# Kernel tuning notes

Measured on AMD Instinct MI355X. Metric: run time of the kernel, lower is better.

The kernel has to match this reference:

```python
import jax, jax.numpy as jnp
import numpy as np

B, S, E, H = 4, 1024, 1024, 16
D = E // H  # head dim = 64

def setup_inputs() -> dict:
    key = jax.random.key(0)
    k1, k2, k3, k4, k5 = jax.random.split(key, 5)
    return {
        "lstm_out": jax.random.normal(k1, (B, S, E), dtype=jnp.float32),
        "in_proj_weight": jax.random.normal(k2, (3 * E, E), dtype=jnp.float32) * 0.02,
        "in_proj_bias": jax.random.normal(k3, (3 * E,), dtype=jnp.float32) * 0.02,
        "out_proj_weight": jax.random.normal(k4, (E, E), dtype=jnp.float32) * 0.02,
        "out_proj_bias": jax.random.normal(k5, (E,), dtype=jnp.float32) * 0.02,
    }

def reference(lstm_out, in_proj_weight, in_proj_bias, out_proj_weight, out_proj_bias):
    # Packed QKV projection, as in nn.MultiheadAttention (Linear uses x @ W.T + b)
    qkv = lstm_out @ in_proj_weight.T + in_proj_bias          # [B,S,3E]
    q, k, v = jnp.split(qkv, 3, axis=-1)                      # each [B,S,E]
    def heads(t):
        return t.reshape(B, S, H, D).transpose(0, 2, 1, 3)    # [B,H,S,D]
    q, k, v = heads(q), heads(k), heads(v)
    scale = 1.0 / jnp.sqrt(jnp.asarray(D, dtype=q.dtype))
    scores = jnp.einsum("bhsd,bhtd->bhst", q * scale, k)      # [B,H,S,S]
    attn = jax.nn.softmax(scores, axis=-1)                    # [B,H,S,S]
    ctx = jnp.einsum("bhst,bhtd->bhsd", attn, v)              # [B,H,S,D]
    ctx = ctx.transpose(0, 2, 1, 3).reshape(B, S, E)          # [B,S,E]
    attn_output = ctx @ out_proj_weight.T + out_proj_bias     # [B,S,E]
    # need_weights=True with default average_attn_weights=True -> mean over heads
    attn_weights = attn.mean(axis=1)                          # [B,S,S]
    context_vector = attn_output.mean(axis=1)                 # [B,E]
    return (context_vector, attn_weights)
```

## Files before the change

### kernel.cpp

```cpp
#include <hip/hip_runtime.h>


typedef unsigned short u16;
using s16x8 = __attribute__((ext_vector_type(8))) short;
using f32x4 = __attribute__((ext_vector_type(4))) float;
using u16x4 = __attribute__((ext_vector_type(4))) unsigned short;

#define AS1 __attribute__((address_space(1)))
#define AS3 __attribute__((address_space(3)))

#define QSCALE 0.1803368801111204f

__device__ __forceinline__ u16 f2bf(float f) {
    unsigned u = __float_as_uint(f);
    u += 0x7fffu + ((u >> 16) & 1u);
    return (u16)(u >> 16);
}

__global__ void k_prep(const float* __restrict__ X, const float* __restrict__ W1,
                       const float* __restrict__ W2, const float* __restrict__ bout,
                       u16* __restrict__ Xb, u16* __restrict__ W1b, u16* __restrict__ W2b,
                       float* __restrict__ out) {
    int i = blockIdx.x * blockDim.x + threadIdx.x;
    const float* src; u16* dst; int off;
    if (i < 1048576)       { src = X;  dst = Xb;  off = i; }
    else if (i < 1835008)  { src = W1; dst = W1b; off = i - 1048576; }
    else                   { src = W2; dst = W2b; off = i - 1835008; }
    float4 v = reinterpret_cast<const float4*>(src)[off];
    u16x4 o = { f2bf(v.x), f2bf(v.y), f2bf(v.z), f2bf(v.w) };
    reinterpret_cast<u16x4*>(dst)[off] = o;
    if (i < 4096) out[i] = bout[i & 1023];
}

template<int MODE>
__global__ __launch_bounds__(512) void k_gemm_bt(
    const u16* __restrict__ A, const u16* __restrict__ B,
    const float* __restrict__ bias, u16* __restrict__ C,
    u16* __restrict__ vt, float* __restrict__ outvec) {
    const int K = 1024;
    constexpr int KSLICE = (MODE == 0) ? 1024 : 256;
    const int nbx = gridDim.x;
    const int nwg = nbx * gridDim.y;
    const int bid = blockIdx.y * nbx + blockIdx.x;
    const int per = nwg >> 3;
    const int swz = (bid & 7) * per + (bid >> 3);
    const int n0 = (swz % nbx) * 128, m0 = (swz / nbx) * 128;
    const int kbeg = blockIdx.z * KSLICE, kend = kbeg + KSLICE;
    const int tid = threadIdx.x, lane = tid & 63, w = tid >> 6;
    const int wm = w >> 1, wn = w & 1;
    const int g = lane >> 4, l15 = lane & 15;
    __shared__ __attribute__((aligned(16))) u16 As[2][128 * 64];
    __shared__ __attribute__((aligned(16))) u16 Bs[2][128 * 64];

    f32x4 acc[2][4];
    #pragma unroll
    for (int mi = 0; mi < 2; ++mi)
        #pragma unroll
        for (int nj = 0; nj < 4; ++nj) acc[mi][nj] = (f32x4){0.f, 0.f, 0.f, 0.f};

    auto STAGE = [&](int k0, int sb) {
        #pragma unroll
        for (int r = 0; r < 2; ++r) {
            int c = tid + r * 512;
            int row = c >> 3, j = c & 7;
            int js = j ^ (row & 7);
            __builtin_amdgcn_global_load_lds(
                (AS1 const void*)(A + (size_t)(m0 + row) * K + k0 + js * 8),
                (AS3 void*)(&As[sb][c * 8]), 16, 0, 0);
            __builtin_amdgcn_global_load_lds(
                (AS1 const void*)(B + (size_t)(n0 + row) * K + k0 + js * 8),
                (AS3 void*)(&Bs[sb][c * 8]), 16, 0, 0);
        }
    };

    STAGE(kbeg, 0);
    int buf = 0;
    for (int k0 = kbeg; k0 < kend; k0 += 64) {
        __syncthreads();
        if (k0 + 64 < kend) STAGE(k0 + 64, buf ^ 1);
        #pragma unroll
        for (int kk = 0; kk < 64; kk += 32) {
            const int cx0 = (((kk >> 3) + g) ^ (l15 & 7)) * 8;
            s16x8 av[2], bv[4];
            #pragma unroll
            for (int mi = 0; mi < 2; ++mi)
                av[mi] = *reinterpret_cast<const s16x8*>(
                    &As[buf][(wm * 32 + mi * 16 + l15) * 64 + cx0]);
            #pragma unroll
            for (int nj = 0; nj < 4; ++nj)
                bv[nj] = *reinterpret_cast<const s16x8*>(
                    &Bs[buf][(wn * 64 + nj * 16 + l15) * 64 + cx0]);
            #pragma unroll
            for (int mi = 0; mi < 2; ++mi)
                #pragma unroll
                for (int nj = 0; nj < 4; ++nj)
                    acc[mi][nj] = __builtin_amdgcn_mfma_f32_16x16x32_bf16(av[mi], bv[nj], acc[mi][nj], 0, 0, 0);
        }
        buf ^= 1;
    }

    if constexpr (MODE == 0) {
        #pragma unroll
        for (int nj = 0; nj < 4; ++nj) {
            int n = n0 + wn * 64 + nj * 16 + l15;
            float scale = (n < 1024) ? QSCALE : 1.0f;
            float bvs = bias[n] * scale;
            if (n < 2048) {
                #pragma unroll
                for (int mi = 0; mi < 2; ++mi)
                    #pragma unroll
                    for (int i = 0; i < 4; ++i) {
                        int m = m0 + wm * 32 + mi * 16 + g * 4 + i;
                        C[(size_t)m * 2048 + n] = f2bf(acc[mi][nj][i] * scale + bvs);
                    }
            } else {
                int hd = n - 2048;
                #pragma unroll
                for (int mi = 0; mi < 2; ++mi)
                    #pragma unroll
                    for (int i = 0; i < 4; ++i) {
                        int m = m0 + wm * 32 + mi * 16 + g * 4 + i;
                        int b = m >> 10, t = m & 1023;
                        vt[((size_t)(b * 16 + (hd >> 6)) * 64 + (hd & 63)) * 1024 + t] =
                            f2bf(acc[mi][nj][i] + bvs);
                    }
            }
        }
    } else {
        int b = m0 >> 10;
        #pragma unroll
        for (int nj = 0; nj < 4; ++nj) {
            float s = 0.f;
            #pragma unroll
            for (int mi = 0; mi < 2; ++mi)
                #pragma unroll
                for (int i = 0; i < 4; ++i) s += acc[mi][nj][i];
            s += __shfl_xor(s, 16);
            s += __shfl_xor(s, 32);
            if (g == 0) {
                int n = n0 + wn * 64 + nj * 16 + l15;
                atomicAdd(&outvec[b * 1024 + n], s * (1.0f / 1024.0f));
            }
        }
    }
}

__global__ __launch_bounds__(256, 4) void k_flash(const u16* __restrict__ qk,
                                                  const u16* __restrict__ vt,
                                                  u16* __restrict__ ctx,
                                                  float* __restrict__ ml) {
    const int id = blockIdx.x + 16 * (blockIdx.y + 16 * blockIdx.z);
    const int x = id & 7, kq = id >> 3;
    const int gbh = x * 8 + (kq >> 4);
    const int qt = kq & 15;
    const int b = gbh >> 4, h = gbh & 15;
    const int q0 = qt * 64;
    const int tid = threadIdx.x, lane = tid & 63, w = tid >> 6;
    const int g = lane >> 4, l15 = lane & 15;
    __shared__ __attribute__((aligned(16))) u16 Ks[2][64 * 64];
    __shared__ __attribute__((aligned(16))) u16 Vt[2][64 * 64];
    __shared__ __attribute__((aligned(16))) u16 Ps[4][16 * 64];

    const size_t rowQ = (size_t)(b * 1024 + q0 + w * 16 + l15) * 2048 + h * 64;
    const s16x8 qa0 = *reinterpret_cast<const s16x8*>(qk + rowQ + g * 8);
    const s16x8 qa1 = *reinterpret_cast<const s16x8*>(qk + rowQ + 32 + g * 8);

    const int cA = tid, cB = tid + 256;
    const int rowA = cA >> 3, jA = cA & 7, rowB = cB >> 3, jB = cB & 7;
    const u16* kbase0 = qk + (size_t)(b * 1024) * 2048 + 1024 + h * 64;
    const u16* vtb = vt + (size_t)(b * 16 + h) * 65536;

    __builtin_amdgcn_global_load_lds((AS1 const void*)(kbase0 + (size_t)rowA * 2048 + ((jA ^ (rowA & 7)) * 8)),
                                     (AS3 void*)(&Ks[0][cA * 8]), 16, 0, 0);
    __builtin_amdgcn_global_load_lds((AS1 const void*)(kbase0 + (size_t)rowB * 2048 + ((jB ^ (rowB & 7)) * 8)),
                                     (AS3 void*)(&Ks[0][cB * 8]), 16, 0, 0);
    __builtin_amdgcn_global_load_lds((AS1 const void*)(vtb + (size_t)rowA * 1024 + ((jA ^ (rowA & 7)) * 8)),
                                     (AS3 void*)(&Vt[0][cA * 8]), 16, 0, 0);
    __builtin_amdgcn_global_load_lds((AS1 const void*)(vtb + (size_t)rowB * 1024 + ((jB ^ (rowB & 7)) * 8)),
                                     (AS3 void*)(&Vt[0][cB * 8]), 16, 0, 0);

    f32x4 ctxa[4];
    #pragma unroll
    for (int nj = 0; nj < 4; ++nj) ctxa[nj] = (f32x4){0.f, 0.f, 0.f, 0.f};
    float lsum = 0.f;

    int buf = 0;
    for (int kt = 0; kt < 16; ++kt) {
        __syncthreads();
        if (kt < 15) {
            int t0n = (kt + 1) * 64;
            const u16* kbase = kbase0 + (size_t)t0n * 2048;
            __builtin_amdgcn_global_load_lds((AS1 const void*)(kbase + (size_t)rowA * 2048 + ((jA ^ (rowA & 7)) * 8)),
                                             (AS3 void*)(&Ks[buf ^ 1][cA * 8]), 16, 0, 0);
            __builtin_amdgcn_global_load_lds((AS1 const void*)(kbase + (size_t)rowB * 2048 + ((jB ^ (rowB & 7)) * 8)),
                                             (AS3 void*)(&Ks[buf ^ 1][cB * 8]), 16, 0, 0);
            const u16* vbase = vtb + t0n;
            __builtin_amdgcn_global_load_lds((AS1 const void*)(vbase + (size_t)rowA * 1024 + ((jA ^ (rowA & 7)) * 8)),
                                             (AS3 void*)(&Vt[buf ^ 1][cA * 8]), 16, 0, 0);
            __builtin_amdgcn_global_load_lds((AS1 const void*)(vbase + (size_t)rowB * 1024 + ((jB ^ (rowB & 7)) * 8)),
                                             (AS3 void*)(&Vt[buf ^ 1][cB * 8]), 16, 0, 0);
        }

        f32x4 sc[4];
        #pragma unroll
        for (int tj = 0; tj < 4; ++tj) sc[tj] = (f32x4){0.f, 0.f, 0.f, 0.f};
        __builtin_amdgcn_s_setprio(1);
        #pragma unroll
        for (int kk = 0; kk < 64; kk += 32) {
            s16x8 qa = kk ? qa1 : qa0;
            #pragma unroll
            for (int tj = 0; tj < 4; ++tj) {
                int trow = tj * 16 + l15;
                s16x8 kb = *reinterpret_cast<const s16x8*>(
                    &Ks[buf][trow * 64 + ((((kk >> 3) + g) ^ (trow & 7)) * 8)]);
                sc[tj] = __builtin_amdgcn_mfma_f32_16x16x32_bf16(kb, qa, sc[tj], 0, 0, 0);
            }
        }
        __builtin_amdgcn_s_setprio(0);

        #pragma unroll
        for (int tj = 0; tj < 4; ++tj)
            #pragma unroll
            for (int i = 0; i < 4; ++i) {
                float p = exp2f(sc[tj][i]);
                sc[tj][i] = p;
                lsum += p;
            }

        #pragma unroll
        for (int tj = 0; tj < 4; ++tj) {
            unsigned pk01, pk23;
            asm("v_cvt_pk_bf16_f32 %0, %1, %2" : "=v"(pk01) : "v"(sc[tj][0]), "v"(sc[tj][1]));
            asm("v_cvt_pk_bf16_f32 %0, %1, %2" : "=v"(pk23) : "v"(sc[tj][2]), "v"(sc[tj][3]));
            uint2 pk = { pk01, pk23 };
            *reinterpret_cast<uint2*>(
                &Ps[w][l15 * 64 + (((tj * 2 + (g >> 1)) ^ (l15 & 7)) * 8) + (g & 1) * 4]) = pk;
        }

        __builtin_amdgcn_s_setprio(1);
        #pragma unroll
        for (int kk = 0; kk < 64; kk += 32) {
            s16x8 pa = *reinterpret_cast<const s16x8*>(
                &Ps[w][l15 * 64 + ((((kk >> 3) + g) ^ (l15 & 7)) * 8)]);
            #pragma unroll
            for (int nj = 0; nj < 4; ++nj) {
                int d = nj * 16 + l15;
                s16x8 vb = *reinterpret_cast<const s16x8*>(
                    &Vt[buf][d * 64 + ((((kk >> 3) + g) ^ (d & 7)) * 8)]);
                ctxa[nj] = __builtin_amdgcn_mfma_f32_16x16x32_bf16(pa, vb, ctxa[nj], 0, 0, 0);
            }
        }
        __builtin_amdgcn_s_setprio(0);
        buf ^= 1;
    }

    lsum += __shfl_xor(lsum, 16);
    lsum += __shfl_xor(lsum, 32);
    float invl = 1.0f / lsum;
    if (g == 0)
        ml[(size_t)(b * 16 + h) * 1024 + q0 + w * 16 + l15] = invl * 0.0625f;

    float invl_i[4];
    #pragma unroll
    for (int i = 0; i < 4; ++i) invl_i[i] = __shfl(invl, g * 4 + i);

    #pragma unroll
    for (int i = 0; i < 4; ++i) {
        int row = q0 + w * 16 + g * 4 + i;
        #pragma unroll
        for (int nj = 0; nj < 4; ++nj) {
            int d = nj * 16 + l15;
            ctx[(size_t)(b * 1024 + row) * 1024 + h * 64 + d] = f2bf(ctxa[nj][i] * invl_i[i]);
        }
    }
}

__global__ __launch_bounds__(256, 4) void k_attnw(const u16* __restrict__ qk,
                                                  const float* __restrict__ ml,
                                                  float* __restrict__ attnw) {
    const int tt = blockIdx.x, st = blockIdx.y, b = blockIdx.z;
    const int s0 = st * 64, t0 = tt * 64;
    const int tid = threadIdx.x, lane = tid & 63, w = tid >> 6;
    const int g = lane >> 4, l15 = lane & 15;
    __shared__ __attribute__((aligned(16))) u16 Ks[2][64 * 64];
    __shared__ float mls[16][64];

    #pragma unroll
    for (int r = 0; r < 4; ++r) {
        int idx = tid + r * 256;
        int hh = idx >> 6, row = idx & 63;
        mls[hh][row] = ml[(size_t)(b * 16 + hh) * 1024 + s0 + row];
    }

    const int cA = tid, cB = tid + 256;
    const int rowA = cA >> 3, jA = cA & 7, rowB = cB >> 3, jB = cB & 7;
    const u16* kbase = qk + (size_t)(b * 1024 + t0) * 2048 + 1024;
    const size_t rowQbase = (size_t)(b * 1024 + s0 + w * 16 + l15) * 2048;

    __builtin_amdgcn_global_load_lds((AS1 const void*)(kbase + (size_t)rowA * 2048 + ((jA ^ (rowA & 7)) * 8)),
                                     (AS3 void*)(&Ks[0][cA * 8]), 16, 0, 0);
    __builtin_amdgcn_global_load_lds((AS1 const void*)(kbase + (size_t)rowB * 2048 + ((jB ^ (rowB & 7)) * 8)),
                                     (AS3 void*)(&Ks[0][cB * 8]), 16, 0, 0);
    s16x8 qc0 = *reinterpret_cast<const s16x8*>(qk + rowQbase + g * 8);
    s16x8 qc1 = *reinterpret_cast<const s16x8*>(qk + rowQbase + 32 + g * 8);

    f32x4 acc[4];
    #pragma unroll
    for (int tj = 0; tj < 4; ++tj) acc[tj] = (f32x4){0.f, 0.f, 0.f, 0.f};

    int buf = 0;
    for (int h = 0; h < 16; ++h) {
        __syncthreads();
        s16x8 qn0, qn1;
        if (h < 15) {
            const u16* kb2 = kbase + (h + 1) * 64;
            __builtin_amdgcn_global_load_lds((AS1 const void*)(kb2 + (size_t)rowA * 2048 + ((jA ^ (rowA & 7)) * 8)),
                                             (AS3 void*)(&Ks[buf ^ 1][cA * 8]), 16, 0, 0);
            __builtin_amdgcn_global_load_lds((AS1 const void*)(kb2 + (size_t)rowB * 2048 + ((jB ^ (rowB & 7)) * 8)),
                                             (AS3 void*)(&Ks[buf ^ 1][cB * 8]), 16, 0, 0);
            qn0 = *reinterpret_cast<const s16x8*>(qk + rowQbase + (h + 1) * 64 + g * 8);
            qn1 = *reinterpret_cast<const s16x8*>(qk + rowQbase + (h + 1) * 64 + 32 + g * 8);
        }

        f32x4 sc[4];
        #pragma unroll
        for (int tj = 0; tj < 4; ++tj) sc[tj] = (f32x4){0.f, 0.f, 0.f, 0.f};
        #pragma unroll
        for (int kk = 0; kk < 64; kk += 32) {
            s16x8 qa = kk ? qc1 : qc0;
            #pragma unroll
            for (int tj = 0; tj < 4; ++tj) {
                int trow = tj * 16 + l15;
                s16x8 kb = *reinterpret_cast<const s16x8*>(
                    &Ks[buf][trow * 64 + ((((kk >> 3) + g) ^ (trow & 7)) * 8)]);
                sc[tj] = __builtin_amdgcn_mfma_f32_16x16x32_bf16(qa, kb, sc[tj], 0, 0, 0);
            }
        }
        #pragma unroll
        for (int i = 0; i < 4; ++i) {
            int row = w * 16 + g * 4 + i;
            float M = mls[h][row];
            #pragma unroll
            for (int tj = 0; tj < 4; ++tj)
                acc[tj][i] += exp2f(fminf(sc[tj][i], 60.f)) * M;
        }
        qc0 = qn0; qc1 = qn1;
        buf ^= 1;
    }

    #pragma unroll
    for (int i = 0; i < 4; ++i) {
        int row = s0 + w * 16 + g * 4 + i;
        #pragma unroll
        for (int tj = 0; tj < 4; ++tj)
            attnw[(size_t)(b * 1024 + row) * 1024 + t0 + tj * 16 + l15] = acc[tj][i];
    }
}

extern "C" void kernel_launch(void* const* d_in, const int* in_sizes, int n_in,
                              void* d_out, int out_size, void* d_ws, size_t ws_size,
                              hipStream_t stream) {
    const float* lstm = (const float*)d_in[0];
    const float* wqkv = (const float*)d_in[1];
    const float* bqkv = (const float*)d_in[2];
    const float* wout = (const float*)d_in[3];
    const float* bout = (const float*)d_in[4];
    float* out = (float*)d_out;

    char* ws = (char*)d_ws;
    u16*   Xbf   = (u16*)(ws);
    u16*   Wqkvb = (u16*)(ws + 8u  * 1024 * 1024);
    u16*   Woutb = (u16*)(ws + 14u * 1024 * 1024);
    u16*   qkbuf = (u16*)(ws + 16u * 1024 * 1024);
    u16*   ctx   = (u16*)(ws + 32u * 1024 * 1024);
    u16*   vtg   = (u16*)(ws + 40u * 1024 * 1024);
    float* ml    = (float*)(ws + 48u * 1024 * 1024);

    k_prep<<<8192, 256, 0, stream>>>(lstm, wqkv, wout, bout, Xbf, Wqkvb, Woutb, out);

    k_gemm_bt<0><<<dim3(24, 32), 512, 0, stream>>>(Xbf, Wqkvb, bqkv, qkbuf, vtg, nullptr);
    k_flash<<<dim3(16, 16, 4), 256, 0, stream>>>(qkbuf, vtg, ctx, ml);
    k_attnw<<<dim3(16, 16, 4), 256, 0, stream>>>(qkbuf, ml, out + 4096);
    k_gemm_bt<1><<<dim3(8, 32, 4), 512, 0, stream>>>(ctx, Woutb, nullptr, nullptr, nullptr, out);
}
```

Measured before the change: 131.8 us.

## Compute softmax row sums via MFMA and double query rows per attnw block

In the flash kernel, the row sum of probabilities is now accumulated with an extra MFMA against a vector of bf16 ones, replacing scalar adds and cross-lane shuffles. This also changes the sum to use bf16-rounded P, matching what multiplies V. The attention-weights kernel now handles 128 query rows per block instead of 64, so each loaded K tile is reused twice and the grid is halved. It also drops the fminf clamp before exp2f. The trade-off is more registers per thread and fewer blocks in the attnw kernel.

```diff
diff --git a/kernel.cpp b/kernel.cpp
--- a/kernel.cpp
+++ b/kernel.cpp
@@ -164,6 +164,8 @@
     const size_t rowQ = (size_t)(b * 1024 + q0 + w * 16 + l15) * 2048 + h * 64;
     const s16x8 qa0 = *reinterpret_cast<const s16x8*>(qk + rowQ + g * 8);
     const s16x8 qa1 = *reinterpret_cast<const s16x8*>(qk + rowQ + 32 + g * 8);
+    const s16x8 onesv = { (short)0x3F80, (short)0x3F80, (short)0x3F80, (short)0x3F80,
+                          (short)0x3F80, (short)0x3F80, (short)0x3F80, (short)0x3F80 };
 
     const int cA = tid, cB = tid + 256;
     const int rowA = cA >> 3, jA = cA & 7, rowB = cB >> 3, jB = cB & 7;
@@ -182,7 +184,7 @@
     f32x4 ctxa[4];
     #pragma unroll
     for (int nj = 0; nj < 4; ++nj) ctxa[nj] = (f32x4){0.f, 0.f, 0.f, 0.f};
-    float lsum = 0.f;
+    f32x4 lacc = (f32x4){0.f, 0.f, 0.f, 0.f};
 
     int buf = 0;
     for (int kt = 0; kt < 16; ++kt) {
@@ -221,11 +223,8 @@
         #pragma unroll
         for (int tj = 0; tj < 4; ++tj)
             #pragma unroll
-            for (int i = 0; i < 4; ++i) {
-                float p = exp2f(sc[tj][i]);
-                sc[tj][i] = p;
-                lsum += p;
-            }
+            for (int i = 0; i < 4; ++i)
+                sc[tj][i] = exp2f(sc[tj][i]);
 
         #pragma unroll
         for (int tj = 0; tj < 4; ++tj) {
@@ -242,6 +241,7 @@
         for (int kk = 0; kk < 64; kk += 32) {
             s16x8 pa = *reinterpret_cast<const s16x8*>(
                 &Ps[w][l15 * 64 + ((((kk >> 3) + g) ^ (l15 & 7)) * 8)]);
+            lacc = __builtin_amdgcn_mfma_f32_16x16x32_bf16(pa, onesv, lacc, 0, 0, 0);
             #pragma unroll
             for (int nj = 0; nj < 4; ++nj) {
                 int d = nj * 16 + l15;
@@ -254,23 +254,16 @@
         buf ^= 1;
     }
 
-    lsum += __shfl_xor(lsum, 16);
-    lsum += __shfl_xor(lsum, 32);
-    float invl = 1.0f / lsum;
-    if (g == 0)
-        ml[(size_t)(b * 16 + h) * 1024 + q0 + w * 16 + l15] = invl * 0.0625f;
-
-    float invl_i[4];
-    #pragma unroll
-    for (int i = 0; i < 4; ++i) invl_i[i] = __shfl(invl, g * 4 + i);
-
     #pragma unroll
     for (int i = 0; i < 4; ++i) {
+        float invl = 1.0f / lacc[i];
         int row = q0 + w * 16 + g * 4 + i;
+        if (l15 == 0)
+            ml[(size_t)(b * 16 + h) * 1024 + row] = invl * 0.0625f;
         #pragma unroll
         for (int nj = 0; nj < 4; ++nj) {
             int d = nj * 16 + l15;
-            ctx[(size_t)(b * 1024 + row) * 1024 + h * 64 + d] = f2bf(ctxa[nj][i] * invl_i[i]);
+            ctx[(size_t)(b * 1024 + row) * 1024 + h * 64 + d] = f2bf(ctxa[nj][i] * invl);
         }
     }
 }
@@ -278,82 +271,100 @@
 __global__ __launch_bounds__(256, 4) void k_attnw(const u16* __restrict__ qk,
                                                   const float* __restrict__ ml,
                                                   float* __restrict__ attnw) {
-    const int tt = blockIdx.x, st = blockIdx.y, b = blockIdx.z;
-    const int s0 = st * 64, t0 = tt * 64;
+    const int tt = blockIdx.x, stp = blockIdx.y, b = blockIdx.z;
+    const int s0a = stp * 128, t0 = tt * 64;
     const int tid = threadIdx.x, lane = tid & 63, w = tid >> 6;
     const int g = lane >> 4, l15 = lane & 15;
     __shared__ __attribute__((aligned(16))) u16 Ks[2][64 * 64];
-    __shared__ float mls[16][64];
-
-    #pragma unroll
-    for (int r = 0; r < 4; ++r) {
+    __shared__ float mls[16][128];
+
+    #pragma unroll
+    for (int r = 0; r < 8; ++r) {
         int idx = tid + r * 256;
-        int hh = idx >> 6, row = idx & 63;
-        mls[hh][row] = ml[(size_t)(b * 16 + hh) * 1024 + s0 + row];
+        int hh = idx >> 7, row = idx & 127;
+        mls[hh][row] = ml[(size_t)(b * 16 + hh) * 1024 + s0a + row];
     }
 
     const int cA = tid, cB = tid + 256;
     const int rowA = cA >> 3, jA = cA & 7, rowB = cB >> 3, jB = cB & 7;
     const u16* kbase = qk + (size_t)(b * 1024 + t0) * 2048 + 1024;
-    const size_t rowQbase = (size_t)(b * 1024 + s0 + w * 16 + l15) * 2048;
+    const size_t rowQa = (size_t)(b * 1024 + s0a + w * 16 + l15) * 2048;
+    const size_t rowQb = rowQa + (size_t)64 * 2048;
 
     __builtin_amdgcn_global_load_lds((AS1 const void*)(kbase + (size_t)rowA * 2048 + ((jA ^ (rowA & 7)) * 8)),
                                      (AS3 void*)(&Ks[0][cA * 8]), 16, 0, 0);
     __builtin_amdgcn_global_load_lds((AS1 const void*)(kbase + (size_t)rowB * 2048 + ((jB ^ (rowB & 7)) * 8)),
                                      (AS3 void*)(&Ks[0][cB * 8]), 16, 0, 0);
-    s16x8 qc0 = *reinterpret_cast<const s16x8*>(qk + rowQbase + g * 8);
-    s16x8 qc1 = *reinterpret_cast<const s16x8*>(qk + rowQbase + 32 + g * 8);
-
-    f32x4 acc[4];
-    #pragma unroll
-    for (int tj = 0; tj < 4; ++tj) acc[tj] = (f32x4){0.f, 0.f, 0.f, 0.f};
+    s16x8 qcA0 = *reinterpret_cast<const s16x8*>(qk + rowQa + g * 8);
+    s16x8 qcA1 = *reinterpret_cast<const s16x8*>(qk + rowQa + 32 + g * 8);
+    s16x8 qcB0 = *reinterpret_cast<const s16x8*>(qk + rowQb + g * 8);
+    s16x8 qcB1 = *reinterpret_cast<const s16x8*>(qk + rowQb + 32 + g * 8);
+
+    f32x4 accA[4], accB[4];
+    #pragma unroll
+    for (int tj = 0; tj < 4; ++tj) {
+        accA[tj] = (f32x4){0.f, 0.f, 0.f, 0.f};
+        accB[tj] = (f32x4){0.f, 0.f, 0.f, 0.f};
+    }
 
     int buf = 0;
     for (int h = 0; h < 16; ++h) {
         __syncthreads();
-        s16x8 qn0, qn1;
+        s16x8 qnA0, qnA1, qnB0, qnB1;
         if (h < 15) {
             const u16* kb2 = kbase + (h + 1) * 64;
             __builtin_amdgcn_global_load_lds((AS1 const void*)(kb2 + (size_t)rowA * 2048 + ((jA ^ (rowA & 7)) * 8)),
                                              (AS3 void*)(&Ks[buf ^ 1][cA * 8]), 16, 0, 0);
             __builtin_amdgcn_global_load_lds((AS1 const void*)(kb2 + (size_t)rowB * 2048 + ((jB ^ (rowB & 7)) * 8)),
                                              (AS3 void*)(&Ks[buf ^ 1][cB * 8]), 16, 0, 0);
-            qn0 = *reinterpret_cast<const s16x8*>(qk + rowQbase + (h + 1) * 64 + g * 8);
-            qn1 = *reinterpret_cast<const s16x8*>(qk + rowQbase + (h + 1) * 64 + 32 + g * 8);
-        }
-
-        f32x4 sc[4];
-        #pragma unroll
-        for (int tj = 0; tj < 4; ++tj) sc[tj] = (f32x4){0.f, 0.f, 0.f, 0.f};
+            qnA0 = *reinterpret_cast<const s16x8*>(qk + rowQa + (h + 1) * 64 + g * 8);
+            qnA1 = *reinterpret_cast<const s16x8*>(qk + rowQa + (h + 1) * 64 + 32 + g * 8);
+            qnB0 = *reinterpret_cast<const s16x8*>(qk + rowQb + (h + 1) * 64 + g * 8);
+            qnB1 = *reinterpret_cast<const s16x8*>(qk + rowQb + (h + 1) * 64 + 32 + g * 8);
+        }
+
+        f32x4 scA[4], scB[4];
+        #pragma unroll
+        for (int tj = 0; tj < 4; ++tj) {
+            scA[tj] = (f32x4){0.f, 0.f, 0.f, 0.f};
+            scB[tj] = (f32x4){0.f, 0.f, 0.f, 0.f};
+        }
         #pragma unroll
         for (int kk = 0; kk < 64; kk += 32) {
-            s16x8 qa = kk ? qc1 : qc0;
+            s16x8 qaA = kk ? qcA1 : qcA0;
+            s16x8 qaB = kk ? qcB1 : qcB0;
             #pragma unroll
             for (int tj = 0; tj < 4; ++tj) {
                 int trow = tj * 16 + l15;
                 s16x8 kb = *reinterpret_cast<const s16x8*>(
                     &Ks[buf][trow * 64 + ((((kk >> 3) + g) ^ (trow & 7)) * 8)]);
-                sc[tj] = __builtin_amdgcn_mfma_f32_16x16x32_bf16(qa, kb, sc[tj], 0, 0, 0);
+                scA[tj] = __builtin_amdgcn_mfma_f32_16x16x32_bf16(qaA, kb, scA[tj], 0, 0, 0);
+                scB[tj] = __builtin_amdgcn_mfma_f32_16x16x32_bf16(qaB, kb, scB[tj], 0, 0, 0);
             }
         }
         #pragma unroll
         for (int i = 0; i < 4; ++i) {
             int row = w * 16 + g * 4 + i;
-            float M = mls[h][row];
-            #pragma unroll
-            for (int tj = 0; tj < 4; ++tj)
-                acc[tj][i] += exp2f(fminf(sc[tj][i], 60.f)) * M;
-        }
-        qc0 = qn0; qc1 = qn1;
+            float Ma = mls[h][row];
+            float Mb = mls[h][64 + row];
+            #pragma unroll
+            for (int tj = 0; tj < 4; ++tj) {
+                accA[tj][i] += exp2f(scA[tj][i]) * Ma;
+                accB[tj][i] += exp2f(scB[tj][i]) * Mb;
+            }
+        }
+        qcA0 = qnA0; qcA1 = qnA1; qcB0 = qnB0; qcB1 = qnB1;
         buf ^= 1;
     }
 
     #pragma unroll
     for (int i = 0; i < 4; ++i) {
-        int row = s0 + w * 16 + g * 4 + i;
-        #pragma unroll
-        for (int tj = 0; tj < 4; ++tj)
-            attnw[(size_t)(b * 1024 + row) * 1024 + t0 + tj * 16 + l15] = acc[tj][i];
+        int rowa = s0a + w * 16 + g * 4 + i;
+        #pragma unroll
+        for (int tj = 0; tj < 4; ++tj) {
+            attnw[(size_t)(b * 1024 + rowa) * 1024 + t0 + tj * 16 + l15] = accA[tj][i];
+            attnw[(size_t)(b * 1024 + rowa + 64) * 1024 + t0 + tj * 16 + l15] = accB[tj][i];
+        }
     }
 }
 
@@ -380,6 +391,6 @@
 
     k_gemm_bt<0><<<dim3(24, 32), 512, 0, stream>>>(Xbf, Wqkvb, bqkv, qkbuf, vtg, nullptr);
     k_flash<<<dim3(16, 16, 4), 256, 0, stream>>>(qkbuf, vtg, ctx, ml);
-    k_attnw<<<dim3(16, 16, 4), 256, 0, stream>>>(qkbuf, ml, out + 4096);
+    k_attnw<<<dim3(16, 8, 4), 256, 0, stream>>>(qkbuf, ml, out + 4096);
     k_gemm_bt<1><<<dim3(8, 32, 4), 512, 0, stream>>>(ctx, Woutb, nullptr, nullptr, nullptr, out);
 }
```

Result: faster. 127.2 us (-3.6%).
